# Performance work log

Hardware: AMD Instinct MI355X
Metric: run time of the kernel (lower is better)

## Reference

```python
import jax, jax.numpy as jnp
import numpy as np
from jax.ops import segment_sum, segment_max

N_USERS = 50000
N_ITEMS = 30000
N_ENTITIES = 80000
D = 64
KG_HOPS = 2        # context_hops / KG_layers
LGCN_LAYERS = 2    # n_layers
TEMP = 0.2
N_KG_EDGES = 2_000_000
N_INTERACT = 1_000_000
N_ADJ = 2_000_000
EPS_PD = 1e-6      # torch PairwiseDistance default eps


def _normalize(x):
    # F.normalize(x, p=2, dim=-1)
    n = jnp.linalg.norm(x, axis=-1, keepdims=True)
    return x / jnp.clip(n, 1e-12)


def _spmm(rows, cols, vals, x, n_rows):
    # sparse (n_rows x k) @ dense (k x d) via gather + segment_sum
    return segment_sum(vals[:, None] * x[cols], rows, num_segments=n_rows)


def setup_inputs() -> dict:
    key = jax.random.key(0)
    ks = jax.random.split(key, 9)
    all_embed = jax.random.normal(ks[0], (N_USERS + N_ENTITIES, D), dtype=jnp.float32) * 0.1
    interact_vals = jax.random.uniform(ks[1], (N_INTERACT,), dtype=jnp.float32)
    adj_vals = jax.random.uniform(ks[2], (N_ADJ,), dtype=jnp.float32)
    edge_index = jax.random.randint(ks[3], (2, N_KG_EDGES), 0, N_ENTITIES, dtype=jnp.int32)
    edge_type = jax.random.randint(ks[4], (N_KG_EDGES,), 0, 32, dtype=jnp.int32)
    interact_rows = jnp.sort(jax.random.randint(ks[5], (N_INTERACT,), 0, N_USERS, dtype=jnp.int32))
    interact_cols = jax.random.randint(ks[6], (N_INTERACT,), 0, N_ITEMS, dtype=jnp.int32)
    adj_rows = jax.random.randint(ks[7], (N_ADJ,), 0, N_USERS + N_ITEMS, dtype=jnp.int32)
    adj_cols = jax.random.randint(ks[8], (N_ADJ,), 0, N_USERS + N_ITEMS, dtype=jnp.int32)
    return {
        "all_embed": all_embed,
        "interact_vals": interact_vals,
        "adj_vals": adj_vals,
        "edge_index": edge_index,
        "edge_type": edge_type,
        "interact_rows": interact_rows,
        "interact_cols": interact_cols,
        "adj_rows": adj_rows,
        "adj_cols": adj_cols,
    }


def _forward(all_embed, interact_vals, adj_vals, edge_index, interact_rows,
             interact_cols, adj_rows, adj_cols):
    user_emb = all_embed[:N_USERS]
    entity_emb = all_embed[N_USERS:]
    head, tail = edge_index[0], edge_index[1]

    u_res, e_res = user_emb, entity_emb
    u, e = user_emb, entity_emb
    ones = jnp.ones((head.shape[0],), dtype=entity_emb.dtype)
    cnt = jnp.clip(segment_sum(ones, head, num_segments=N_ENTITIES), 1.0)

    for _ in range(KG_HOPS):
        # scatter_mean KG aggregation: entity_agg[h] = mean over tails of edges with head h
        entity_agg = segment_sum(e[tail], head, num_segments=N_ENTITIES) / cnt[:, None]
        item_agg = entity_agg[:N_ITEMS]
        # user_mean = interact_map @ entity_agg[:n_items]
        user_mean = _spmm(interact_rows, interact_cols, interact_vals, item_agg, N_USERS)
        # pairwise L2 distance per interaction nnz
        diff = item_agg[interact_cols] - user_mean[interact_rows] + EPS_PD
        score = jnp.linalg.norm(diff, axis=-1) / TEMP
        # sparse softmax over rows (users)
        m = segment_max(score, interact_rows, num_segments=N_USERS)
        ex = jnp.exp(score - m[interact_rows])
        denom = segment_sum(ex, interact_rows, num_segments=N_USERS)
        att = ex / denom[interact_rows]
        # user_agg = sparse.mm(soft_score_mat, item_agg)
        user_agg = segment_sum(att[:, None] * item_agg[interact_cols],
                               interact_rows, num_segments=N_USERS)
        e = _normalize(entity_agg)
        u = _normalize(user_agg)
        e_res = e_res + e
        u_res = u_res + u

    # LightGCN over bipartite graph
    x = jnp.concatenate([u_res, e_res[:N_ITEMS]], axis=0)  # [n_users+n_items, D]
    acc = x
    for _ in range(LGCN_LAYERS):
        x = _spmm(adj_rows, adj_cols, adj_vals, x, N_USERS + N_ITEMS)
        acc = acc + x
    out = acc / float(LGCN_LAYERS + 1)
    return out[:N_USERS], out[N_USERS:]


def reference(all_embed, interact_vals, adj_vals, edge_index, edge_type,
              interact_rows, interact_cols, adj_rows, adj_cols):
    # edge_type is passed through the original forward but unused by Aggregator
    return _forward(all_embed, interact_vals, adj_vals, edge_index,
                    interact_rows, interact_cols, adj_rows, adj_cols)
```

## Files before the change

kernel.cpp:

```cpp
#include <hip/hip_runtime.h>
#include <math.h>

#define N_USERS 50000
#define N_ITEMS 30000
#define N_ENTITIES 80000
#define N_UI (N_USERS + N_ITEMS)
#define D 64
#define N_KG_EDGES 2000000
#define N_INTERACT 1000000
#define N_ADJ 2000000
#define INV_TEMP 5.0f
#define EPS_PD 1e-6f
#define SHIFT 7
#define NB 625
#define BKEYS 128
#define BMASK 127
#define EPB 8192
#define BIG 1024
#define GRID_EP 245
#define UH_GRID 12500
#define KG2_GRID 7500
#define CVT_GRID 1875

typedef _Float16 f16;
typedef unsigned short u16;

__device__ __forceinline__ float4 ld_h4(const f16* p) {
    struct h4 { f16 x, y, z, w; };
    h4 h = *(const h4*)p;
    return make_float4((float)h.x, (float)h.y, (float)h.z, (float)h.w);
}

__device__ __forceinline__ void st_h4(f16* p, float4 v) {
    struct h4 { f16 x, y, z, w; };
    h4 h = {(f16)v.x, (f16)v.y, (f16)v.z, (f16)v.w};
    *(h4*)p = h;
}

__device__ __forceinline__ u16 f16_bits(float v) {
    f16 h = (f16)v;
    return __builtin_bit_cast(u16, h);
}

__device__ __forceinline__ float bits_f16(unsigned b) {
    return (float)__builtin_bit_cast(f16, (u16)b);
}

__global__ void stageA(const int* __restrict__ kg_ei, const int* __restrict__ adj_r,
                       const int* __restrict__ irows, int* __restrict__ bcntK,
                       int* __restrict__ bcntA, int* __restrict__ rowstart) {
    __shared__ int h[NB];
    int bb = blockIdx.x;
    if (bb < 2 * GRID_EP) {
        bool kg = bb < GRID_EP;
        const int* keys = kg ? kg_ei : adj_r;
        int* bcnt = kg ? bcntK : bcntA;
        int blk = kg ? bb : bb - GRID_EP;
        int n = kg ? N_KG_EDGES : N_ADJ;
        for (int i = threadIdx.x; i < NB; i += BIG) h[i] = 0;
        __syncthreads();
        int e0 = blk * EPB, e1 = min(e0 + EPB, n);
        for (int e = e0 + (int)threadIdx.x; e < e1; e += BIG)
            atomicAdd(&h[keys[e] >> SHIFT], 1);
        __syncthreads();
        for (int i = threadIdx.x; i < NB; i += BIG)
            if (h[i]) atomicAdd(&bcnt[i], h[i]);
    } else {
        int r = (bb - 2 * GRID_EP) * BIG + threadIdx.x;
        if (r > N_USERS) return;
        int lo = 0, hi = N_INTERACT;
        while (lo < hi) {
            int mid = (lo + hi) >> 1;
            if (irows[mid] < r) lo = mid + 1; else hi = mid;
        }
        rowstart[r] = lo;
    }
}

__global__ void bscan_both(const int* __restrict__ cntK, int* __restrict__ boffK,
                           int* __restrict__ bcurK, const int* __restrict__ cntA,
                           int* __restrict__ boffA, int* __restrict__ bcurA) {
    __shared__ int wp[4];
    __shared__ int carry_s;
    const int* cnt = blockIdx.x ? cntA : cntK;
    int* boff = blockIdx.x ? boffA : boffK;
    int* bcur = blockIdx.x ? bcurA : bcurK;
    int lane = threadIdx.x & 63, wv = threadIdx.x >> 6;
    if (threadIdx.x == 0) { carry_s = 0; boff[0] = 0; }
    __syncthreads();
    for (int base = 0; base < NB; base += 256) {
        int i = base + (int)threadIdx.x;
        int v = (i < NB) ? cnt[i] : 0;
        int x = v;
        #pragma unroll
        for (int o = 1; o < 64; o <<= 1) {
            int t = __shfl_up(x, o, 64);
            if (lane >= o) x += t;
        }
        if (lane == 63) wp[wv] = x;
        __syncthreads();
        int add = carry_s;
        for (int j = 0; j < wv; ++j) add += wp[j];
        int incl = x + add;
        if (i < NB) { boff[i + 1] = incl; bcur[i] = incl - v; }
        __syncthreads();
        if (threadIdx.x == 255) carry_s = incl;
        __syncthreads();
    }
}

__global__ void binA_both(const int* __restrict__ kg_ei, int* __restrict__ bcurK,
                          int* __restrict__ kg_bin, const int* __restrict__ adj_r,
                          const int* __restrict__ adj_c, const float* __restrict__ adj_v,
                          int* __restrict__ bcurA, int2* __restrict__ rc) {
    __shared__ int hist[NB], base[NB];
    bool kg = blockIdx.x < GRID_EP;
    int blk = kg ? blockIdx.x : blockIdx.x - GRID_EP;
    int n = kg ? N_KG_EDGES : N_ADJ;
    int* bcur = kg ? bcurK : bcurA;
    const int* keys = kg ? kg_ei : adj_r;
    for (int i = threadIdx.x; i < NB; i += BIG) hist[i] = 0;
    __syncthreads();
    int e0 = blk * EPB;
    for (int i = threadIdx.x; i < EPB; i += BIG) {
        int e = e0 + i;
        if (e < n) atomicAdd(&hist[keys[e] >> SHIFT], 1);
    }
    __syncthreads();
    for (int b = threadIdx.x; b < NB; b += BIG)
        base[b] = hist[b] ? atomicAdd(&bcur[b], hist[b]) : 0;
    __syncthreads();
    for (int i = threadIdx.x; i < NB; i += BIG) hist[i] = 0;
    __syncthreads();
    for (int i = threadIdx.x; i < EPB; i += BIG) {
        int e = e0 + i;
        if (e >= n) continue;
        int k = keys[e];
        int b = k >> SHIFT;
        int slot = base[b] + atomicAdd(&hist[b], 1);
        if (kg) kg_bin[slot] = (kg_ei[n + e] << SHIFT) | (k & BMASK);
        else    rc[slot] = make_int2((adj_c[e] << SHIFT) | (k & BMASK),
                                     __float_as_int(adj_v[e]));
    }
}

__global__ void binC_both(const int* __restrict__ boffK, const int* __restrict__ kg_bin,
                          int* __restrict__ tails, int* __restrict__ rowptrK,
                          float* __restrict__ icnt, const int* __restrict__ boffA,
                          const int2* __restrict__ rc, int* __restrict__ pair,
                          int* __restrict__ rowptrA) {
    __shared__ int cnt_s[BKEYS];
    __shared__ int cur_s[BKEYS];
    __shared__ int wp2[2];
    bool kg = blockIdx.x < NB;
    int b = kg ? blockIdx.x : blockIdx.x - NB;
    const int* boff = kg ? boffK : boffA;
    int k0 = b << SHIFT;
    int s = boff[b], t = boff[b + 1];
    if (threadIdx.x < BKEYS) cnt_s[threadIdx.x] = 0;
    __syncthreads();
    for (int i = s + (int)threadIdx.x; i < t; i += 256)
        atomicAdd(&cnt_s[(kg ? kg_bin[i] : rc[i].x) & BMASK], 1);
    __syncthreads();
    int lane = threadIdx.x & 63, wv = threadIdx.x >> 6;
    int v = (threadIdx.x < BKEYS) ? cnt_s[threadIdx.x] : 0;
    int x = v;
    #pragma unroll
    for (int o = 1; o < 64; o <<= 1) {
        int tt = __shfl_up(x, o, 64);
        if (lane >= o) x += tt;
    }
    if (threadIdx.x < BKEYS && lane == 63) wp2[wv] = x;
    __syncthreads();
    int add = (wv == 1) ? wp2[0] : 0;
    int excl = s + (x - v) + add;
    if (threadIdx.x < BKEYS) {
        cur_s[threadIdx.x] = excl;
        if (kg) {
            rowptrK[k0 + threadIdx.x] = excl;
            icnt[k0 + threadIdx.x] = 1.0f / fmaxf((float)v, 1.0f);
        } else {
            rowptrA[k0 + threadIdx.x] = excl;
        }
    }
    if (threadIdx.x == 0 && b == NB - 1) {
        if (kg) rowptrK[N_ENTITIES] = t; else rowptrA[N_UI] = t;
    }
    __syncthreads();
    if (kg) {
        for (int i = s + (int)threadIdx.x; i < t; i += 256) {
            int p = kg_bin[i];
            int slot = atomicAdd(&cur_s[p & BMASK], 1);
            tails[slot] = (unsigned)p >> SHIFT;
        }
    } else {
        for (int i = s + (int)threadIdx.x; i < t; i += 256) {
            int2 p = rc[i];
            int slot = atomicAdd(&cur_s[p.x & BMASK], 1);
            unsigned col = (unsigned)p.x >> SHIFT;
            unsigned vb = f16_bits(__int_as_float(p.y)) & 0x7FFFu;
            pair[slot] = (int)((col << 15) | vb);
        }
    }
}

template <bool FIRST>
__device__ __forceinline__ void kg_hop_body(
        int wid, const int* __restrict__ rowptr, const int* __restrict__ tails,
        const float* __restrict__ icnt, const float* __restrict__ Ain,
        float* __restrict__ Aout, float* __restrict__ ER,
        const float* __restrict__ ERI, float* __restrict__ snorm, int nrows) {
    int lane = threadIdx.x & 63;
    int g = lane >> 4, gl = lane & 15;
    if (wid >= nrows) return;
    int s = rowptr[wid], t = rowptr[wid + 1];
    float4 acc = {0.f, 0.f, 0.f, 0.f};
    for (int e = s + g; e < t; e += 16) {
        int e1 = e + 4, e2 = e + 8, e3 = e + 12;
        int c0 = tails[e];
        int c1 = (e1 < t) ? tails[e1] : 0;
        int c2 = (e2 < t) ? tails[e2] : 0;
        int c3 = (e3 < t) ? tails[e3] : 0;
        float4 r0 = *(const float4*)(Ain + (size_t)c0 * D + gl * 4);
        float4 r1 = {0.f, 0.f, 0.f, 0.f};
        float4 r2 = {0.f, 0.f, 0.f, 0.f};
        float4 r3 = {0.f, 0.f, 0.f, 0.f};
        if (e1 < t) r1 = *(const float4*)(Ain + (size_t)c1 * D + gl * 4);
        if (e2 < t) r2 = *(const float4*)(Ain + (size_t)c2 * D + gl * 4);
        if (e3 < t) r3 = *(const float4*)(Ain + (size_t)c3 * D + gl * 4);
        acc.x += (r0.x + r1.x) + (r2.x + r3.x);
        acc.y += (r0.y + r1.y) + (r2.y + r3.y);
        acc.z += (r0.z + r1.z) + (r2.z + r3.z);
        acc.w += (r0.w + r1.w) + (r2.w + r3.w);
    }
    acc.x += __shfl_xor(acc.x, 16, 64); acc.x += __shfl_xor(acc.x, 32, 64);
    acc.y += __shfl_xor(acc.y, 16, 64); acc.y += __shfl_xor(acc.y, 32, 64);
    acc.z += __shfl_xor(acc.z, 16, 64); acc.z += __shfl_xor(acc.z, 32, 64);
    acc.w += __shfl_xor(acc.w, 16, 64); acc.w += __shfl_xor(acc.w, 32, 64);
    float ss = acc.x * acc.x + acc.y * acc.y + acc.z * acc.z + acc.w * acc.w;
    ss += __shfl_xor(ss, 1, 64); ss += __shfl_xor(ss, 2, 64);
    ss += __shfl_xor(ss, 4, 64); ss += __shfl_xor(ss, 8, 64);
    float nrm = fmaxf(sqrtf(ss), 1e-12f);
    float inv = 1.0f / nrm;
    if (g == 0) {
        size_t o = (size_t)wid * D + gl * 4;
        float4 ev = {acc.x * inv, acc.y * inv, acc.z * inv, acc.w * inv};
        *(float4*)(Aout + o) = ev;
        if (wid < N_ITEMS) {
            float4 er = FIRST ? *(const float4*)(ERI + o) : *(const float4*)(ER + o);
            er.x += ev.x; er.y += ev.y; er.z += ev.z; er.w += ev.w;
            *(float4*)(ER + o) = er;
            if (gl == 0) snorm[wid] = nrm * icnt[wid];
        }
    }
}

template <bool FIRST>
__device__ __forceinline__ void user_hop_body(
        int wid, const float* __restrict__ E, const float* __restrict__ snorm,
        const int* __restrict__ rowstart, const int* __restrict__ cols,
        const float* __restrict__ vals, float* __restrict__ UR,
        const float* __restrict__ URI, f16* __restrict__ XHu) {
    int lane = threadIdx.x & 63;
    int g = lane >> 4, gl = lane & 15;
    if (wid >= N_USERS) return;
    int s = rowstart[wid], t = rowstart[wid + 1];

    float4 mean = {0.f, 0.f, 0.f, 0.f};
    #define UH_LOAD(K)                                                          \
        const int eP##K = s + g + 4 * K;                                        \
        const bool ok##K = eP##K < t;                                           \
        const int cP##K = ok##K ? cols[eP##K] : 0;                              \
        const float snP##K = ok##K ? snorm[cP##K] : 0.f;                        \
        const float vP##K = ok##K ? vals[eP##K] : 0.f;                          \
        float4 rP##K = {0.f, 0.f, 0.f, 0.f};                                    \
        if (ok##K) rP##K = *(const float4*)(E + (size_t)cP##K * D + gl * 4);
    UH_LOAD(0) UH_LOAD(1) UH_LOAD(2) UH_LOAD(3) UH_LOAD(4) UH_LOAD(5)
    #undef UH_LOAD
    #define UH_MEAN(K) {                                                        \
        float w = vP##K * snP##K;                                               \
        mean.x += w * rP##K.x; mean.y += w * rP##K.y;                           \
        mean.z += w * rP##K.z; mean.w += w * rP##K.w; }
    UH_MEAN(0) UH_MEAN(1) UH_MEAN(2) UH_MEAN(3) UH_MEAN(4) UH_MEAN(5)
    #undef UH_MEAN
    for (int e = s + g + 24; e < t; e += 4) {
        int c = cols[e];
        float w = vals[e] * snorm[c];
        float4 r = *(const float4*)(E + (size_t)c * D + gl * 4);
        mean.x += w * r.x; mean.y += w * r.y;
        mean.z += w * r.z; mean.w += w * r.w;
    }
    mean.x += __shfl_xor(mean.x, 16, 64); mean.x += __shfl_xor(mean.x, 32, 64);
    mean.y += __shfl_xor(mean.y, 16, 64); mean.y += __shfl_xor(mean.y, 32, 64);
    mean.z += __shfl_xor(mean.z, 16, 64); mean.z += __shfl_xor(mean.z, 32, 64);
    mean.w += __shfl_xor(mean.w, 16, 64); mean.w += __shfl_xor(mean.w, 32, 64);

    float4 b = {mean.x - EPS_PD, mean.y - EPS_PD, mean.z - EPS_PD, mean.w - EPS_PD};
    float bb = b.x * b.x + b.y * b.y + b.z * b.z + b.w * b.w;
    bb += __shfl_xor(bb, 1, 64); bb += __shfl_xor(bb, 2, 64);
    bb += __shfl_xor(bb, 4, 64); bb += __shfl_xor(bb, 8, 64);

    float m = -INFINITY, denom = 0.f;
    float4 acc = {0.f, 0.f, 0.f, 0.f};
    #define UH_SM(K) if (ok##K) {                                               \
        float dl = rP##K.x * b.x + rP##K.y * b.y + rP##K.z * b.z + rP##K.w * b.w; \
        dl += __shfl_xor(dl, 1, 64); dl += __shfl_xor(dl, 2, 64);               \
        dl += __shfl_xor(dl, 4, 64); dl += __shfl_xor(dl, 8, 64);               \
        float s2 = fmaxf(snP##K * snP##K - 2.f * snP##K * dl + bb, 0.f);        \
        float sc = sqrtf(s2) * INV_TEMP;                                        \
        float dlt = sc - m;                                                     \
        float tt = __expf(fminf(dlt, -dlt));                                    \
        bool up = dlt > 0.f;                                                    \
        float scale = up ? tt : 1.f;                                            \
        float ex = up ? 1.f : tt;                                               \
        if (up) m = sc;                                                         \
        denom = denom * scale + ex;                                             \
        float w = ex * snP##K;                                                  \
        acc.x = acc.x * scale + w * rP##K.x;                                    \
        acc.y = acc.y * scale + w * rP##K.y;                                    \
        acc.z = acc.z * scale + w * rP##K.z;                                    \
        acc.w = acc.w * scale + w * rP##K.w; }
    UH_SM(0) UH_SM(1) UH_SM(2) UH_SM(3) UH_SM(4) UH_SM(5)
    #undef UH_SM
    for (int e = s + g + 24; e < t; e += 4) {
        int c = cols[e];
        float sn = snorm[c];
        float4 r = *(const float4*)(E + (size_t)c * D + gl * 4);
        float dl = r.x * b.x + r.y * b.y + r.z * b.z + r.w * b.w;
        dl += __shfl_xor(dl, 1, 64); dl += __shfl_xor(dl, 2, 64);
        dl += __shfl_xor(dl, 4, 64); dl += __shfl_xor(dl, 8, 64);
        float s2 = fmaxf(sn * sn - 2.f * sn * dl + bb, 0.f);
        float sc = sqrtf(s2) * INV_TEMP;
        float dlt = sc - m;
        float tt = __expf(fminf(dlt, -dlt));
        bool up = dlt > 0.f;
        float scale = up ? tt : 1.f;
        float ex = up ? 1.f : tt;
        if (up) m = sc;
        denom = denom * scale + ex;
        float w = ex * sn;
        acc.x = acc.x * scale + w * r.x;
        acc.y = acc.y * scale + w * r.y;
        acc.z = acc.z * scale + w * r.z;
        acc.w = acc.w * scale + w * r.w;
    }
    float mg = fmaxf(m, __shfl_xor(m, 16, 64));
    mg = fmaxf(mg, __shfl_xor(mg, 32, 64));
    float scl = __expf(fmaxf(m - mg, -88.0f));
    denom *= scl;
    acc.x *= scl; acc.y *= scl; acc.z *= scl; acc.w *= scl;
    denom += __shfl_xor(denom, 16, 64); denom += __shfl_xor(denom, 32, 64);
    acc.x += __shfl_xor(acc.x, 16, 64); acc.x += __shfl_xor(acc.x, 32, 64);
    acc.y += __shfl_xor(acc.y, 16, 64); acc.y += __shfl_xor(acc.y, 32, 64);
    acc.z += __shfl_xor(acc.z, 16, 64); acc.z += __shfl_xor(acc.z, 32, 64);
    acc.w += __shfl_xor(acc.w, 16, 64); acc.w += __shfl_xor(acc.w, 32, 64);
    float invd = denom > 0.f ? 1.0f / denom : 0.f;
    acc.x *= invd; acc.y *= invd; acc.z *= invd; acc.w *= invd;
    float ss = acc.x * acc.x + acc.y * acc.y + acc.z * acc.z + acc.w * acc.w;
    ss += __shfl_xor(ss, 1, 64); ss += __shfl_xor(ss, 2, 64);
    ss += __shfl_xor(ss, 4, 64); ss += __shfl_xor(ss, 8, 64);
    float inv = 1.0f / fmaxf(sqrtf(ss), 1e-12f);
    if (g == 0) {
        size_t o = (size_t)wid * D + gl * 4;
        float4 u = FIRST ? *(const float4*)(URI + o) : *(const float4*)(UR + o);
        u.x += acc.x * inv; u.y += acc.y * inv; u.z += acc.z * inv; u.w += acc.w * inv;
        *(float4*)(UR + o) = u;
        if (XHu) st_h4(XHu + o, u);
    }
}

__global__ void kg1_kernel(const int* __restrict__ rowptr, const int* __restrict__ tails,
                           const float* __restrict__ icnt, const float* __restrict__ Ain,
                           float* __restrict__ A1, float* __restrict__ ER,
                           const float* __restrict__ ERI, float* __restrict__ sn1) {
    int wid = (blockIdx.x * blockDim.x + threadIdx.x) >> 6;
    kg_hop_body<true>(wid, rowptr, tails, icnt, Ain, A1, ER, ERI, sn1, N_ENTITIES);
}

__global__ void mid_kernel(const float* __restrict__ A1, const float* __restrict__ sn1,
                           const int* __restrict__ rowstart, const int* __restrict__ cols,
                           const float* __restrict__ vals, float* __restrict__ UR,
                           const float* __restrict__ URI, const int* __restrict__ rowptr,
                           const int* __restrict__ tails, const float* __restrict__ icnt,
                           float* __restrict__ A0I, float* __restrict__ ER,
                           float* __restrict__ sn2) {
    if (blockIdx.x < UH_GRID) {
        int wid = (blockIdx.x * blockDim.x + threadIdx.x) >> 6;
        user_hop_body<true>(wid, A1, sn1, rowstart, cols, vals, UR, URI, nullptr);
    } else {
        int wid = (((blockIdx.x - UH_GRID) * blockDim.x) + threadIdx.x) >> 6;
        kg_hop_body<false>(wid, rowptr, tails, icnt, A1, A0I, ER, nullptr, sn2, N_ITEMS);
    }
}

__global__ void fin_kernel(const float* __restrict__ A0I, const float* __restrict__ sn2,
                           const int* __restrict__ rowstart, const int* __restrict__ cols,
                           const float* __restrict__ vals, float* __restrict__ UR,
                           f16* __restrict__ XH, const float* __restrict__ ER) {
    if (blockIdx.x < UH_GRID) {
        int wid = (blockIdx.x * blockDim.x + threadIdx.x) >> 6;
        user_hop_body<false>(wid, A0I, sn2, rowstart, cols, vals, UR, nullptr, XH);
    } else {
        int i = (blockIdx.x - UH_GRID) * blockDim.x + threadIdx.x;
        if (i < (N_ITEMS * D) / 4)
            st_h4(XH + (size_t)N_USERS * D + (size_t)i * 4,
                  *(const float4*)(ER + (size_t)i * 4));
    }
}

__device__ __forceinline__ const float* xrow32(const float* U, const float* I, int c) {
    return (c < N_USERS) ? (U + (size_t)c * D) : (I + (size_t)(c - N_USERS) * D);
}

template <int MODE>
__global__ void adj_spmm(const int* __restrict__ rowptr, const int* __restrict__ pair,
                         const f16* __restrict__ X, const float* __restrict__ XAU,
                         const float* __restrict__ XAI, f16* __restrict__ Y,
                         float* __restrict__ out) {
    int wid = (blockIdx.x * blockDim.x + threadIdx.x) >> 6;
    int lane = threadIdx.x & 63;
    int g = lane >> 4, gl = lane & 15;
    if (wid >= N_UI) return;
    int s = rowptr[wid], t = rowptr[wid + 1];
    float4 acc = {0.f, 0.f, 0.f, 0.f};
    for (int e = s + g; e < t; e += 16) {
        int e1 = e + 4, e2 = e + 8, e3 = e + 12;
        int p0 = pair[e];
        int p1 = (e1 < t) ? pair[e1] : 0;
        int p2 = (e2 < t) ? pair[e2] : 0;
        int p3 = (e3 < t) ? pair[e3] : 0;
        float4 r0 = ld_h4(X + (size_t)((unsigned)p0 >> 15) * D + gl * 4);
        float4 r1 = {0.f, 0.f, 0.f, 0.f};
        float4 r2 = {0.f, 0.f, 0.f, 0.f};
        float4 r3 = {0.f, 0.f, 0.f, 0.f};
        if (e1 < t) r1 = ld_h4(X + (size_t)((unsigned)p1 >> 15) * D + gl * 4);
        if (e2 < t) r2 = ld_h4(X + (size_t)((unsigned)p2 >> 15) * D + gl * 4);
        if (e3 < t) r3 = ld_h4(X + (size_t)((unsigned)p3 >> 15) * D + gl * 4);
        float v0 = bits_f16(p0 & 0x7FFF), v1 = bits_f16(p1 & 0x7FFF);
        float v2 = bits_f16(p2 & 0x7FFF), v3 = bits_f16(p3 & 0x7FFF);
        acc.x += (v0 * r0.x + v1 * r1.x) + (v2 * r2.x + v3 * r3.x);
        acc.y += (v0 * r0.y + v1 * r1.y) + (v2 * r2.y + v3 * r3.y);
        acc.z += (v0 * r0.z + v1 * r1.z) + (v2 * r2.z + v3 * r3.z);
        acc.w += (v0 * r0.w + v1 * r1.w) + (v2 * r2.w + v3 * r3.w);
    }
    acc.x += __shfl_xor(acc.x, 16, 64); acc.x += __shfl_xor(acc.x, 32, 64);
    acc.y += __shfl_xor(acc.y, 16, 64); acc.y += __shfl_xor(acc.y, 32, 64);
    acc.z += __shfl_xor(acc.z, 16, 64); acc.z += __shfl_xor(acc.z, 32, 64);
    acc.w += __shfl_xor(acc.w, 16, 64); acc.w += __shfl_xor(acc.w, 32, 64);
    if (g == 0) {
        size_t o = (size_t)wid * D + gl * 4;
        if (MODE == 0) {
            st_h4(Y + o, acc);
            const float4 xa = *(const float4*)(xrow32(XAU, XAI, wid) + gl * 4);
            float4 ov = {xa.x + acc.x, xa.y + acc.y, xa.z + acc.z, xa.w + acc.w};
            *(float4*)(out + o) = ov;
        } else {
            float4 ov = *(const float4*)(out + o);
            ov.x = (ov.x + acc.x) * (1.0f / 3.0f);
            ov.y = (ov.y + acc.y) * (1.0f / 3.0f);
            ov.z = (ov.z + acc.z) * (1.0f / 3.0f);
            ov.w = (ov.w + acc.w) * (1.0f / 3.0f);
            *(float4*)(out + o) = ov;
        }
    }
}

extern "C" void kernel_launch(void* const* d_in, const int* in_sizes, int n_in,
                              void* d_out, int out_size, void* d_ws, size_t ws_size,
                              hipStream_t stream) {
    const float* all_embed     = (const float*)d_in[0];
    const float* interact_vals = (const float*)d_in[1];
    const float* adj_vals      = (const float*)d_in[2];
    const int*   edge_index    = (const int*)d_in[3];
    const int*   interact_rows = (const int*)d_in[5];
    const int*   interact_cols = (const int*)d_in[6];
    const int*   adj_rows      = (const int*)d_in[7];
    const int*   adj_cols      = (const int*)d_in[8];
    float* out = (float*)d_out;

    const size_t usrN = (size_t)N_USERS * D;
    const size_t itmN = (size_t)N_ITEMS * D;
    const size_t entN = (size_t)N_ENTITIES * D;

    float* cur = (float*)d_ws;
    float* UR  = cur; cur += usrN;
    float* ER  = cur; cur += itmN;
    float* A0I = cur; cur += itmN;
    float* A1  = cur; cur += entN;
    int*  KG_TAIL  = (int*)cur; cur += N_KG_EDGES;
    int*  ADJ_PAIR = (int*)cur; cur += N_ADJ;
    float* ICNT   = cur; cur += N_ENTITIES;
    float* SNORM1 = cur; cur += N_ITEMS + 16;
    float* SNORM2 = cur; cur += N_ITEMS + 16;
    int* KG_ROWPTR  = (int*)cur;
    int* ADJ_ROWPTR = KG_ROWPTR + N_ENTITIES + 2;
    int* BCNT_K     = ADJ_ROWPTR + N_UI + 2;
    int* BCNT_A     = BCNT_K + NB;
    int* BOFF_K     = BCNT_A + NB;
    int* BOFF_A     = BOFF_K + NB + 1;
    int* BCUR_K     = BOFF_A + NB + 1;
    int* BCUR_A     = BCUR_K + NB;
    int* ROWSTART   = BCUR_A + NB;

    int*  KG_BIN = (int*)UR;
    int2* ADJ_RC = (int2*)A1;
    f16*  XH  = (f16*)A1;
    f16*  X1H = XH + (size_t)N_UI * D;

    hipMemsetAsync(BCNT_K, 0, 2 * NB * sizeof(int), stream);
    stageA<<<2 * GRID_EP + 49, BIG, 0, stream>>>(edge_index, adj_rows, interact_rows,
                                                 BCNT_K, BCNT_A, ROWSTART);
    bscan_both<<<2, 256, 0, stream>>>(BCNT_K, BOFF_K, BCUR_K, BCNT_A, BOFF_A, BCUR_A);
    binA_both<<<2 * GRID_EP, BIG, 0, stream>>>(edge_index, BCUR_K, KG_BIN, adj_rows,
                                               adj_cols, adj_vals, BCUR_A, ADJ_RC);
    binC_both<<<2 * NB, 256, 0, stream>>>(BOFF_K, KG_BIN, KG_TAIL, KG_ROWPTR, ICNT,
                                          BOFF_A, ADJ_RC, ADJ_PAIR, ADJ_ROWPTR);

    kg1_kernel<<<N_ENTITIES / 4, 256, 0, stream>>>(KG_ROWPTR, KG_TAIL, ICNT,
                                                   all_embed + usrN, A1, ER,
                                                   all_embed + usrN, SNORM1);
    mid_kernel<<<UH_GRID + KG2_GRID, 256, 0, stream>>>(A1, SNORM1, ROWSTART,
                                                       interact_cols, interact_vals,
                                                       UR, all_embed, KG_ROWPTR, KG_TAIL,
                                                       ICNT, A0I, ER, SNORM2);
    fin_kernel<<<UH_GRID + CVT_GRID, 256, 0, stream>>>(A0I, SNORM2, ROWSTART,
                                                       interact_cols, interact_vals,
                                                       UR, XH, ER);

    adj_spmm<0><<<N_UI / 4, 256, 0, stream>>>(ADJ_ROWPTR, ADJ_PAIR, XH, UR, ER, X1H, out);
    adj_spmm<1><<<N_UI / 4, 256, 0, stream>>>(ADJ_ROWPTR, ADJ_PAIR, X1H, nullptr, nullptr,
                                              nullptr, out);
}
```

Before: 388.6 us.

## Stage binned edges in shared memory and pack adjacency payload before scatter

```diff
diff --git a/kernel.cpp b/kernel.cpp
--- a/kernel.cpp
+++ b/kernel.cpp
@@ -24,6 +24,7 @@
 
 typedef _Float16 f16;
 typedef unsigned short u16;
+typedef unsigned char u8;
 
 __device__ __forceinline__ float4 ld_h4(const f16* p) {
     struct h4 { f16 x, y, z, w; };
@@ -112,43 +113,92 @@
 __global__ void binA_both(const int* __restrict__ kg_ei, int* __restrict__ bcurK,
                           int* __restrict__ kg_bin, const int* __restrict__ adj_r,
                           const int* __restrict__ adj_c, const float* __restrict__ adj_v,
-                          int* __restrict__ bcurA, int2* __restrict__ rc) {
-    __shared__ int hist[NB], base[NB];
+                          int* __restrict__ bcurA, int* __restrict__ rcP,
+                          u8* __restrict__ rcK) {
+    __shared__ int stage4[EPB];
+    __shared__ u8 stageK[EPB];
+    __shared__ int histS[NB], lstartS[NB], gbaseS[NB];
+    __shared__ int wpS[16];
     bool kg = blockIdx.x < GRID_EP;
     int blk = kg ? blockIdx.x : blockIdx.x - GRID_EP;
     int n = kg ? N_KG_EDGES : N_ADJ;
     int* bcur = kg ? bcurK : bcurA;
     const int* keys = kg ? kg_ei : adj_r;
-    for (int i = threadIdx.x; i < NB; i += BIG) hist[i] = 0;
+    int tid = threadIdx.x;
+    if (tid < NB) histS[tid] = 0;
     __syncthreads();
     int e0 = blk * EPB;
-    for (int i = threadIdx.x; i < EPB; i += BIG) {
+    for (int i = tid; i < EPB; i += BIG) {
         int e = e0 + i;
-        if (e < n) atomicAdd(&hist[keys[e] >> SHIFT], 1);
-    }
-    __syncthreads();
-    for (int b = threadIdx.x; b < NB; b += BIG)
-        base[b] = hist[b] ? atomicAdd(&bcur[b], hist[b]) : 0;
-    __syncthreads();
-    for (int i = threadIdx.x; i < NB; i += BIG) hist[i] = 0;
-    __syncthreads();
-    for (int i = threadIdx.x; i < EPB; i += BIG) {
+        if (e < n) atomicAdd(&histS[keys[e] >> SHIFT], 1);
+    }
+    __syncthreads();
+    {
+        int lane = tid & 63, wv = tid >> 6;
+        int v = (tid < NB) ? histS[tid] : 0;
+        int x = v;
+        #pragma unroll
+        for (int o = 1; o < 64; o <<= 1) {
+            int t = __shfl_up(x, o, 64);
+            if (lane >= o) x += t;
+        }
+        if (lane == 63) wpS[wv] = x;
+        __syncthreads();
+        if (wv == 0) {
+            int p = (lane < 16) ? wpS[lane] : 0;
+            #pragma unroll
+            for (int o = 1; o < 16; o <<= 1) {
+                int t = __shfl_up(p, o, 64);
+                if (lane >= o) p += t;
+            }
+            if (lane < 16) wpS[lane] = p;
+        }
+        __syncthreads();
+        int add = (wv > 0) ? wpS[wv - 1] : 0;
+        if (tid < NB) {
+            lstartS[tid] = (x - v) + add;
+            gbaseS[tid] = v ? atomicAdd(&bcur[tid], v) : 0;
+            histS[tid] = 0;
+        }
+    }
+    __syncthreads();
+    for (int i = tid; i < EPB; i += BIG) {
         int e = e0 + i;
         if (e >= n) continue;
         int k = keys[e];
         int b = k >> SHIFT;
-        int slot = base[b] + atomicAdd(&hist[b], 1);
-        if (kg) kg_bin[slot] = (kg_ei[n + e] << SHIFT) | (k & BMASK);
-        else    rc[slot] = make_int2((adj_c[e] << SHIFT) | (k & BMASK),
-                                     __float_as_int(adj_v[e]));
+        int slot = lstartS[b] + atomicAdd(&histS[b], 1);
+        if (kg) {
+            stage4[slot] = (kg_ei[n + e] << SHIFT) | (k & BMASK);
+        } else {
+            stage4[slot] = (adj_c[e] << 15) | (int)(f16_bits(adj_v[e]) & 0x7FFFu);
+            stageK[slot] = (u8)(k & BMASK);
+        }
+    }
+    __syncthreads();
+    {
+        int lane = tid & 63, wv = tid >> 6;
+        for (int b = wv; b < NB; b += 16) {
+            int nb = histS[b];
+            int src = lstartS[b], dst = gbaseS[b];
+            if (kg) {
+                for (int j = lane; j < nb; j += 64)
+                    kg_bin[dst + j] = stage4[src + j];
+            } else {
+                for (int j = lane; j < nb; j += 64) {
+                    rcP[dst + j] = stage4[src + j];
+                    rcK[dst + j] = stageK[src + j];
+                }
+            }
+        }
     }
 }
 
 __global__ void binC_both(const int* __restrict__ boffK, const int* __restrict__ kg_bin,
                           int* __restrict__ tails, int* __restrict__ rowptrK,
                           float* __restrict__ icnt, const int* __restrict__ boffA,
-                          const int2* __restrict__ rc, int* __restrict__ pair,
-                          int* __restrict__ rowptrA) {
+                          const int* __restrict__ rcP, const u8* __restrict__ rcK,
+                          int* __restrict__ pair, int* __restrict__ rowptrA) {
     __shared__ int cnt_s[BKEYS];
     __shared__ int cur_s[BKEYS];
     __shared__ int wp2[2];
@@ -160,7 +210,7 @@
     if (threadIdx.x < BKEYS) cnt_s[threadIdx.x] = 0;
     __syncthreads();
     for (int i = s + (int)threadIdx.x; i < t; i += 256)
-        atomicAdd(&cnt_s[(kg ? kg_bin[i] : rc[i].x) & BMASK], 1);
+        atomicAdd(&cnt_s[kg ? (kg_bin[i] & BMASK) : (int)rcK[i]], 1);
     __syncthreads();
     int lane = threadIdx.x & 63, wv = threadIdx.x >> 6;
     int v = (threadIdx.x < BKEYS) ? cnt_s[threadIdx.x] : 0;
@@ -195,11 +245,8 @@
         }
     } else {
         for (int i = s + (int)threadIdx.x; i < t; i += 256) {
-            int2 p = rc[i];
-            int slot = atomicAdd(&cur_s[p.x & BMASK], 1);
-            unsigned col = (unsigned)p.x >> SHIFT;
-            unsigned vb = f16_bits(__int_as_float(p.y)) & 0x7FFFu;
-            pair[slot] = (int)((col << 15) | vb);
+            int slot = atomicAdd(&cur_s[(int)rcK[i]], 1);
+            pair[slot] = rcP[i];
         }
     }
 }
@@ -502,19 +549,22 @@
     int* BCUR_A     = BCUR_K + NB;
     int* ROWSTART   = BCUR_A + NB;
 
-    int*  KG_BIN = (int*)UR;
-    int2* ADJ_RC = (int2*)A1;
-    f16*  XH  = (f16*)A1;
-    f16*  X1H = XH + (size_t)N_UI * D;
+    int* KG_BIN = (int*)UR;
+    int* ADJ_RCP = (int*)A1;
+    u8*  ADJ_RCK = (u8*)(A1 + N_ADJ);
+    f16* XH  = (f16*)A1;
+    f16* X1H = XH + (size_t)N_UI * D;
 
     hipMemsetAsync(BCNT_K, 0, 2 * NB * sizeof(int), stream);
     stageA<<<2 * GRID_EP + 49, BIG, 0, stream>>>(edge_index, adj_rows, interact_rows,
                                                  BCNT_K, BCNT_A, ROWSTART);
     bscan_both<<<2, 256, 0, stream>>>(BCNT_K, BOFF_K, BCUR_K, BCNT_A, BOFF_A, BCUR_A);
     binA_both<<<2 * GRID_EP, BIG, 0, stream>>>(edge_index, BCUR_K, KG_BIN, adj_rows,
-                                               adj_cols, adj_vals, BCUR_A, ADJ_RC);
+                                               adj_cols, adj_vals, BCUR_A,
+                                               ADJ_RCP, ADJ_RCK);
     binC_both<<<2 * NB, 256, 0, stream>>>(BOFF_K, KG_BIN, KG_TAIL, KG_ROWPTR, ICNT,
-                                          BOFF_A, ADJ_RC, ADJ_PAIR, ADJ_ROWPTR);
+                                          BOFF_A, ADJ_RCP, ADJ_RCK, ADJ_PAIR,
+                                          ADJ_ROWPTR);
 
     kg1_kernel<<<N_ENTITIES / 4, 256, 0, stream>>>(KG_ROWPTR, KG_TAIL, ICNT,
                                                    all_embed + usrN, A1, ER,
```

Measured after the change: 375.4 us, median of 2. 3.4% less time.
